# Kernel tuning notes

Measured on AMD Instinct MI355X. Metric: run time of the kernel, lower is better.

Reference implementation:

```python
import jax, jax.numpy as jnp
import numpy as np
from jax.scipy.special import logsumexp

NG, NF, NR, NW = 5, 5, 5, 4
STEP = 1 + NG + NF + NR            # 16 signatures per writer
M_OTH = NG + NF + NR               # comparisons per writer
MARGIN, RANDOM_MARGIN = 1.0, 1.5
ALPHA, BETA, P_W, R_W = 0.1, 1.0, 0.01, 0.01
GAMMA = 5.0                        # SoftDTW(gamma=5, bandwidth=int(0.1)=0 -> full DTW)
KNUM, KMUL = 5, 2.0
MAXLEN, FEAT = 512, 64
BIG = 1e10                         # finite stand-in for +inf (exp(-BIG/GAMMA) == 0 in f32)


def _pairwise_sqdist(X, Y):
    # X,Y: (B, L, F) -> (B, L, L) squared euclidean cost (SoftDTW distance func)
    xy = jnp.einsum('bif,bjf->bij', X, Y)
    d = (X * X).sum(-1)[:, :, None] + (Y * Y).sum(-1)[:, None, :] - 2.0 * xy
    return jnp.maximum(d, 0.0)


def _soft_dtw(D, la, lb):
    # Batched soft-DTW via anti-diagonal scan. Padded DP is causal, so
    # R[la, lb] only depends on D[:la, :lb]; padding never contaminates it.
    B, L, _ = D.shape
    ii = jnp.arange(1, L + 1)
    r2 = jnp.full((B, L + 1), BIG, D.dtype).at[:, 0].set(0.0)  # diag d=0: R[0,0]=0
    r1 = jnp.full((B, L + 1), BIG, D.dtype)                    # diag d=1: borders

    def step(carry, d):
        rp2, rp1 = carry
        j = d - ii
        valid = (j >= 1) & (j <= L)
        jc = jnp.clip(j, 1, L)
        Dd = D[:, ii - 1, jc - 1]                               # (B, L)
        # softmin(R[i-1,j], R[i,j-1], R[i-1,j-1]) = -g*logsumexp(-r/g)
        stack = jnp.stack([-rp1[:, :-1], -rp1[:, 1:], -rp2[:, :-1]]) / GAMMA
        smin = -GAMMA * logsumexp(stack, axis=0)
        vals = jnp.where(valid[None, :], Dd + smin, BIG)
        r_new = jnp.concatenate([jnp.full((B, 1), BIG, D.dtype), vals], axis=1)
        return (rp1, r_new), r_new

    _, R = jax.lax.scan(step, (r2, r1), jnp.arange(2, 2 * L + 1))
    # R: (2L-1, B, L+1); diag d stored at d-2, R[la, lb] sits at index la
    return R[la + lb - 2, jnp.arange(B), la]


def _mmd(src, tgt):
    # DAN-style multi-kernel gaussian MMD; signatures flattened to vectors
    b = src.shape[0]
    total = jnp.concatenate([src, tgt], axis=0)
    n = total.shape[0]
    sq = (total * total).sum(-1)
    l2 = jnp.maximum(sq[:, None] + sq[None, :] - 2.0 * (total @ total.T), 0.0)
    bw = jax.lax.stop_gradient(l2.sum()) / (n * n - n)
    bw = bw / KMUL ** (KNUM // 2)
    bws = bw * KMUL ** jnp.arange(KNUM, dtype=total.dtype)
    k = jnp.exp(-l2[None] / bws[:, None, None]).sum(0)
    return jnp.mean(k[:b, :b] + k[b:, b:] - k[:b, b:] - k[b:, :b])


def _forward(data, lens):
    w = jnp.arange(NW)
    anchor_idx = jnp.repeat(w * STEP, M_OTH)
    other_idx = (w[:, None] * STEP + 1 + jnp.arange(M_OTH)[None, :]).reshape(-1)
    D = _pairwise_sqdist(data[anchor_idx], data[other_idx])
    la, lb = lens[anchor_idx], lens[other_idx]
    r = _soft_dtw(D, la, lb)
    dists = (r / (la + lb).astype(data.dtype)).reshape(NW, M_OTH)  # avg pooling
    dist_g = dists[:, :NG]
    dist_n = dists[:, NG:]
    lk_s = jax.nn.relu(dist_g[:, :, None] + MARGIN - dist_n[:, None, :NF])
    lk_r = jax.nn.relu(dist_g[:, :, None] + RANDOM_MARGIN - dist_n[:, None, NF:])
    ca = dist_g.mean(1)
    cb = dist_n[:, :NW].mean(1)            # quirk of original: first nw negatives
    intra = (dist_g - ca[:, None]).sum(1)  # identically 0, kept for fidelity
    inter = jax.nn.relu(BETA - jnp.abs(ca - cb))
    nz_s = (lk_s > 0).sum((1, 2))
    nz_r = (lk_r > 0).sum((1, 2))
    lv = (lk_s.sum((1, 2)) + lk_r.sum((1, 2))) / (nz_s + nz_r + 1)
    # BCE over softmin pairs (dist_g[0], dist_r[j]) vs targets (1, 0):
    # softmin gives sm0 = sigmoid(dr - dg0); BCE = -(log sm0 + log(1-sm1))/2 = -log sm0
    logits = dist_n[:, NF:] - dist_g[:, 0:1]
    bce = -jnp.mean(jax.nn.log_sigmoid(logits), axis=1)
    total_loss = jnp.mean(bce + lv + intra * P_W + inter * R_W)
    # pairwise MMD over writers (i in 0..nw-1, j in 1..nw-1, i != j), nr random excluded
    pairs = np.array([(i, j) for i in range(NW) for j in range(1, NW) if i != j])
    seg = data.reshape(NW, STEP, MAXLEN, FEAT)[:, :STEP - NR]
    seg = seg.reshape(NW, STEP - NR, MAXLEN * FEAT)
    mmd_vals = jax.vmap(_mmd)(seg[pairs[:, 0]], seg[pairs[:, 1]])
    siz = NW * (NW + 1) // 2
    mmds = jnp.zeros((siz,), data.dtype).at[:pairs.shape[0]].set(mmd_vals)
    mmd1 = jnp.max(mmds) * ALPHA
    return total_loss + mmd1, nz_r.sum()


def setup_inputs():
    key = jax.random.key(0)
    k1, k2, k3 = jax.random.split(key, 3)
    data = jax.random.normal(k1, (NW * STEP, MAXLEN, FEAT), dtype=jnp.float32)
    lens = jax.random.randint(k2, (NW * STEP,), MAXLEN // 2, MAXLEN + 1, dtype=jnp.int32)
    target = jax.random.randint(k3, (NW * STEP,), 0, NW, dtype=jnp.int32)
    return {"data": data, "lens": lens, "target": target, "n_classes": 100}


def reference(data, lens, target, n_classes):
    # target / n_classes are unused in the original forward (sms is dead code)
    return _forward(data, lens)
```

## Files before the change

kernel.cpp:

```cpp
#include <hip/hip_runtime.h>
#include <math.h>

#define NG 5
#define NF 5
#define NR 5
#define NW 4
#define STEP 16
#define M_OTH 15
#define NB 60
#define L 512
#define FEAT 64
#define GAMMA 5.0f
#define SEGN 11
#define NSEG 44
#define SEGD 32768

#define C1   0.28853900817779268f
#define GLN2 3.4657359027997265f
#define BIGS 2.8853900e9f
#define BNDW 800
#define GRAM_BLK0 60
#define SENT 0x7FC000007FC00000ULL

typedef struct __align__(16) { unsigned long long x, y; } ull2_t;

__global__ __launch_bounds__(256, 2) void sqdist_kernel(const float* __restrict__ data,
                                                        const int* __restrict__ lens,
                                                        float* __restrict__ DS) {
    int b = blockIdx.z;
    int w = b / M_OTH, m = b % M_OTH;
    int la = lens[w * STEP];
    int lb = lens[w * STEP + 1 + m];
    int ti = blockIdx.y * 128;
    int tj = blockIdx.x * 128;
    if (ti >= la || tj >= lb) return;

    const float* X = data + (size_t)(w * STEP) * L * FEAT;
    const float* Y = data + (size_t)(w * STEP + 1 + m) * L * FEAT;

    __shared__ float Xs[128][68];
    __shared__ float Ys[128][68];
    __shared__ float nx[128], ny[128];

    int t = threadIdx.y * 16 + threadIdx.x;
    #pragma unroll
    for (int k = 0; k < 8; ++k) {
        int idx = t + k * 256;
        int r = idx >> 4, c = (idx & 15) * 4;
        *(float4*)&Xs[r][c] = *(const float4*)(X + (size_t)(ti + r) * FEAT + c);
        *(float4*)&Ys[r][c] = *(const float4*)(Y + (size_t)(tj + r) * FEAT + c);
    }
    __syncthreads();
    {
        int r = t & 127;
        const float* row = (t < 128) ? Xs[r] : Ys[r];
        float s = 0.f;
        #pragma unroll
        for (int f = 0; f < 64; f += 4) {
            float4 v = *(const float4*)&row[f];
            s += v.x * v.x + v.y * v.y + v.z * v.z + v.w * v.w;
        }
        if (t < 128) nx[r] = s; else ny[r] = s;
    }
    __syncthreads();

    int tx = threadIdx.x, ty = threadIdx.y;
    float acc[8][8] = {};
    for (int f = 0; f < 64; f += 4) {
        float4 xv[8], yv[8];
        #pragma unroll
        for (int a = 0; a < 8; ++a) xv[a] = *(const float4*)&Xs[16 * a + tx][f];
        #pragma unroll
        for (int c = 0; c < 8; ++c) yv[c] = *(const float4*)&Ys[16 * c + ty][f];
        #pragma unroll
        for (int a = 0; a < 8; ++a)
            #pragma unroll
            for (int c = 0; c < 8; ++c)
                acc[a][c] += xv[a].x * yv[c].x + xv[a].y * yv[c].y +
                             xv[a].z * yv[c].z + xv[a].w * yv[c].w;
    }
    #pragma unroll
    for (int a = 0; a < 8; ++a) {
        int ii = ti + 16 * a + tx;
        float xn = nx[16 * a + tx];
        #pragma unroll
        for (int c = 0; c < 8; ++c) {
            int jj = tj + 16 * c + ty;
            float d = xn + ny[16 * c + ty] - 2.0f * acc[a][c];
            size_t idx = ((size_t)b * 512 + ((jj + (ii >> 1)) & 511)) * 512 + ii;
            DS[idx] = fmaxf(d, 0.0f) * C1;
        }
    }
}

__device__ __forceinline__ float dpp_shift_up1(float x) {
    int xi = __float_as_int(x);
    int sh  = __builtin_amdgcn_update_dpp(xi, xi, 0x111, 0xF, 0xF, false);
    int b15 = __builtin_amdgcn_update_dpp(xi, xi, 0x142, 0xF, 0xF, false);
    int lane = (int)(threadIdx.x & 63);
    int r = ((lane & 15) == 0) ? b15 : sh;
    return __int_as_float(r);
}

__device__ void gram_body(const float* __restrict__ data, float* __restrict__ Gm, int f) {
    int bx = 0, rem = f;
    for (int q = 0; q < 11; ++q) { int c = 11 - q; if (rem < c) { bx = q; break; } rem -= c; }
    int by = bx + rem;
    int t = threadIdx.x;
    int lane = t & 63, wv = t >> 6;
    const float* pa[4];
    const float* pb[4];
    #pragma unroll
    for (int i = 0; i < 4; ++i) {
        int sa = bx * 4 + i;
        int sb = by * 4 + i;
        pa[i] = data + (size_t)((sa / SEGN) * STEP + (sa % SEGN)) * SEGD;
        pb[i] = data + (size_t)((sb / SEGN) * STEP + (sb % SEGN)) * SEGD;
    }
    float acc[16] = {};
    for (int d = t * 4; d < SEGD; d += 1024) {
        float4 ra[4], rb[4];
        #pragma unroll
        for (int i = 0; i < 4; ++i) ra[i] = *(const float4*)(pa[i] + d);
        #pragma unroll
        for (int i = 0; i < 4; ++i) rb[i] = *(const float4*)(pb[i] + d);
        #pragma unroll
        for (int i = 0; i < 4; ++i)
            #pragma unroll
            for (int jj = 0; jj < 4; ++jj)
                acc[i * 4 + jj] += ra[i].x * rb[jj].x + ra[i].y * rb[jj].y +
                                   ra[i].z * rb[jj].z + ra[i].w * rb[jj].w;
    }
    #pragma unroll
    for (int i = 0; i < 16; ++i)
        #pragma unroll
        for (int s = 32; s > 0; s >>= 1)
            acc[i] += __shfl_xor(acc[i], s);
    __shared__ float part[4][16];
    if (lane == 0)
        #pragma unroll
        for (int i = 0; i < 16; ++i) part[wv][i] = acc[i];
    __syncthreads();
    if (t < 16) {
        float s = part[0][t] + part[1][t] + part[2][t] + part[3][t];
        int a = bx * 4 + (t >> 2), c = by * 4 + (t & 3);
        Gm[a * NSEG + c] = s;
        Gm[c * NSEG + a] = s;
    }
}

__global__ __launch_bounds__(256) void dtw_gram_kernel(const float* __restrict__ DS,
                                                       const int* __restrict__ lens,
                                                       const float* __restrict__ data,
                                                       float* __restrict__ res,
                                                       float* __restrict__ Gm) {
    int blk = blockIdx.x;
    if (blk >= GRAM_BLK0) { gram_body(data, Gm, blk - GRAM_BLK0); return; }

    int b = blk;
    int w_ = b / M_OTH, m = b % M_OTH;
    int la = lens[w_ * STEP];
    int lb = lens[w_ * STEP + 1 + m];
    int tid = threadIdx.x;
    int W = tid >> 6, l = tid & 63, G = tid;
    const float* Db = DS + (size_t)b * 512 * 512;

    __shared__ unsigned long long bnd[3][BNDW];
    for (int k = tid; k < 3 * BNDW; k += 256)
        ((unsigned long long*)bnd)[k] = SENT;
    __syncthreads();

    int gstar = (la - 1) >> 1;
    int rstar = (la - 1) & 1;
    int tcap = lb + gstar - 1;
    if (64 * W > gstar) return;
    int gmax = min(64 * W + 63, gstar);
    int t0 = 64 * W;
    int tend = lb + gmax - 1;
    int needmax = lb + 64 * W - 1;
    bool pub = (W < 3);

    float p0 = BIGS, s0 = 1.f;
    float p1 = BIGS, s1 = 1.f;
    float pA = BIGS, sA = 1.f;
    float pC = (G == 0) ? 0.f : BIGS;
    float sC = 1.f;
    float outp = 0.f, outs = 1.f;

    float2 ring[8];
    #pragma unroll
    for (int k = 0; k < 8; ++k)
        ring[k] = *(const float2*)&Db[(size_t)((t0 + k) & 511) * 512 + 2 * G];
    unsigned long long ch[8];
    #pragma unroll
    for (int k = 0; k < 8; ++k) ch[k] = SENT;

    int j = 1 - l;
    const unsigned long long* bsrc = (W > 0) ? bnd[W - 1] : bnd[0];

    for (int t = t0; t <= tend; t += 8) {
        if (W > 0 && t <= needmax) {
            bool ok = (t + 7 <= needmax) &&
                      !__builtin_isnan(__int_as_float((int)(unsigned)ch[3])) &&
                      !__builtin_isnan(__int_as_float((int)(unsigned)ch[7]));
            if (!ok) {
                int lastIdx = min(t + 7, needmax);
                unsigned long long v = __hip_atomic_load(&bsrc[lastIdx], __ATOMIC_RELAXED,
                                                         __HIP_MEMORY_SCOPE_WORKGROUP);
                while (__builtin_isnan(__int_as_float((int)(unsigned)v))) {
                    __builtin_amdgcn_s_sleep(2);
                    v = __hip_atomic_load(&bsrc[lastIdx], __ATOMIC_RELAXED,
                                          __HIP_MEMORY_SCOPE_WORKGROUP);
                }
                __builtin_amdgcn_fence(__ATOMIC_ACQUIRE, "workgroup");
                #pragma unroll
                for (int k = 0; k < 8; ++k)
                    ch[k] = __hip_atomic_load(&bsrc[t + k], __ATOMIC_RELAXED,
                                              __HIP_MEMORY_SCOPE_WORKGROUP);
            }
        }
        #pragma unroll
        for (int k = 0; k < 8; ++k) {
            int tt = t + k;
            float l0p = BIGS, l0s = 1.0f;
            if (W > 0 && tt <= needmax) {
                l0p = __int_as_float((int)(unsigned)ch[k]);
                l0s = __int_as_float((int)(unsigned)(ch[k] >> 32));
            }
            pA = (l == 0) ? l0p : pA;
            sA = (l == 0) ? l0s : sA;
            float D0 = ring[k].x, D1 = ring[k].y;
            ring[k] = *(const float2*)&Db[(size_t)((tt + 8) & 511) * 512 + 2 * G];
            float mbc = fminf(p0, pC), xbc = fmaxf(p0, pC);
            float ebc = __builtin_amdgcn_exp2f(mbc - xbc);
            float E2  = (p0 <= pC) ? fmaf(ebc, sC, s0) : fmaf(ebc, s0, sC);
            float ref0 = fminf(pA, mbc), mx0 = fmaxf(pA, mbc);
            float e0 = __builtin_amdgcn_exp2f(ref0 - mx0);
            float s0n = (pA <= mbc) ? fmaf(e0, E2, sA) : fmaf(e0, sA, E2);
            float p0n = D0 + ref0;
            float mbc1 = fminf(p1, p0), xbc1 = fmaxf(p1, p0);
            float ebc1 = __builtin_amdgcn_exp2f(mbc1 - xbc1);
            float E2b = (p1 <= p0) ? fmaf(ebc1, s0, s1) : fmaf(ebc1, s1, s0);
            float ref1 = fminf(p0n, mbc1), mx1 = fmaxf(p0n, mbc1);
            float e1 = __builtin_amdgcn_exp2f(ref1 - mx1);
            float s1n = (p0n <= mbc1) ? fmaf(e1, E2b, s0n) : fmaf(e1, s0n, E2b);
            float p1n = D1 + ref1;
            bool valid = (unsigned)(j - 1) < (unsigned)L;
            p0 = valid ? p0n : p0;  s0 = valid ? s0n : s0;
            p1 = valid ? p1n : p1;  s1 = valid ? s1n : s1;
            if (tt == tcap) {
                if (G == gstar) { outp = rstar ? p1 : p0; outs = rstar ? s1 : s0; }
            }
            float upP = dpp_shift_up1(p1);
            float upS = dpp_shift_up1(s1);
            if (pub && l == 63) {
                union { float2 f; unsigned long long u; } pk;
                pk.f = make_float2(p1, s1);
                __hip_atomic_store(&bnd[W][tt + 1], pk.u, __ATOMIC_RELAXED,
                                   __HIP_MEMORY_SCOPE_WORKGROUP);
            }
            pC = pA; sC = sA;
            pA = upP; sA = upS;
            j += 1;
        }
        if ((t & 8) != 0) {
            p0 -= __builtin_amdgcn_logf(s0); s0 = 1.0f;
            p1 -= __builtin_amdgcn_logf(s1); s1 = 1.0f;
        }
        if (W > 0) {
            const ull2_t* sp = (const ull2_t*)&bsrc[t + 8];
            ull2_t c0 = sp[0], c1 = sp[1], c2 = sp[2], c3 = sp[3];
            ch[0] = c0.x; ch[1] = c0.y; ch[2] = c1.x; ch[3] = c1.y;
            ch[4] = c2.x; ch[5] = c2.y; ch[6] = c3.x; ch[7] = c3.y;
        }
    }
    if (G == gstar)
        res[b] = (outp - __builtin_amdgcn_logf(outs)) * GLN2 / (float)(la + lb);
}

__global__ __launch_bounds__(512) void finalize_kernel(const float* __restrict__ res,
                                                       const float* __restrict__ G,
                                                       float* __restrict__ out) {
    __shared__ float wpart[9][8];
    __shared__ float bws[9];
    __shared__ float mmds[9];
    __shared__ float wloss[NW];
    __shared__ int   wnzr[NW];
    int t = threadIdx.x, lane = t & 63, wv = t >> 6;

    if (t < NW) {
        int w = t;
        float dg[NG], dn[NF + NR];
        for (int g = 0; g < NG; ++g) dg[g] = res[w * M_OTH + g];
        for (int q2 = 0; q2 < NF + NR; ++q2) dn[q2] = res[w * M_OTH + NG + q2];
        float sum_s = 0.f, sum_r = 0.f;
        int nzs = 0, nzr = 0;
        for (int g = 0; g < NG; ++g) {
            for (int f = 0; f < NF; ++f) {
                float v = dg[g] + 1.0f - dn[f];
                if (v > 0.f) { sum_s += v; nzs++; }
            }
            for (int r = 0; r < NR; ++r) {
                float v = dg[g] + 1.5f - dn[NF + r];
                if (v > 0.f) { sum_r += v; nzr++; }
            }
        }
        float ca = (dg[0] + dg[1] + dg[2] + dg[3] + dg[4]) / 5.0f;
        float cb = (dn[0] + dn[1] + dn[2] + dn[3]) * 0.25f;
        float intra = 0.f;
        for (int g = 0; g < NG; ++g) intra += dg[g] - ca;
        float inter = fmaxf(0.f, 1.0f - fabsf(ca - cb));
        float lv = (sum_s + sum_r) / (float)(nzs + nzr + 1);
        float bce = 0.f;
        for (int r = 0; r < NR; ++r) {
            float x = dn[NF + r] - dg[0];
            float ls = (x >= 0.f) ? -log1pf(expf(-x)) : (x - log1pf(expf(x)));
            bce += ls;
        }
        bce = -bce / 5.0f;
        wloss[w] = bce + lv + intra * 0.01f + inter * 0.01f;
        wnzr[w] = nzr;
    }

    const int pi[9] = {0, 0, 0, 1, 1, 2, 2, 3, 3};
    const int pj[9] = {1, 2, 3, 2, 3, 1, 3, 1, 2};
    int pp = t / 22, qq = t % 22;
    bool act = t < 484;
    float l2v[9];
    #pragma unroll
    for (int p = 0; p < 9; ++p) {
        float v = 0.f;
        if (act) {
            int wi = pi[p], wj = pj[p];
            int gp = (pp < 11) ? wi * SEGN + pp : wj * SEGN + (pp - 11);
            int gq = (qq < 11) ? wi * SEGN + qq : wj * SEGN + (qq - 11);
            v = fmaxf(G[gp * NSEG + gp] + G[gq * NSEG + gq] - 2.f * G[gp * NSEG + gq], 0.f);
        }
        l2v[p] = v;
    }
    #pragma unroll
    for (int p = 0; p < 9; ++p) {
        float r = l2v[p];
        #pragma unroll
        for (int s = 32; s > 0; s >>= 1) r += __shfl_xor(r, s);
        if (lane == 0) wpart[p][wv] = r;
    }
    __syncthreads();
    if (t < 9) {
        float s = 0.f;
        #pragma unroll
        for (int k = 0; k < 8; ++k) s += wpart[t][k];
        bws[t] = s * (1.0f / 462.0f) * 0.25f;
    }
    __syncthreads();
    float sgn = ((pp < 11) == (qq < 11)) ? 1.f : -1.f;
    #pragma unroll
    for (int p = 0; p < 9; ++p) {
        float kv = 0.f;
        if (act) {
            float x = -l2v[p] / bws[p];
            kv = sgn * (__expf(x) + __expf(x * 0.5f) + __expf(x * 0.25f) +
                        __expf(x * 0.125f) + __expf(x * 0.0625f));
        }
        #pragma unroll
        for (int s = 32; s > 0; s >>= 1) kv += __shfl_xor(kv, s);
        if (lane == 0) wpart[p][wv] = kv;
    }
    __syncthreads();
    if (t < 9) {
        float s = 0.f;
        #pragma unroll
        for (int k = 0; k < 8; ++k) s += wpart[t][k];
        mmds[t] = s / 121.0f;
    }
    __syncthreads();
    if (t == 0) {
        float loss = 0.25f * (wloss[0] + wloss[1] + wloss[2] + wloss[3]);
        float mx = 0.f;
        for (int p = 0; p < 9; ++p) mx = fmaxf(mx, mmds[p]);
        out[0] = loss + 0.1f * mx;
        out[1] = (float)(wnzr[0] + wnzr[1] + wnzr[2] + wnzr[3]);
    }
}

extern "C" void kernel_launch(void* const* d_in, const int* in_sizes, int n_in,
                              void* d_out, int out_size, void* d_ws, size_t ws_size,
                              hipStream_t stream) {
    const float* data = (const float*)d_in[0];
    const int* lens = (const int*)d_in[1];

    float* DS  = (float*)d_ws;
    float* res = DS + (size_t)NB * 512 * 512;
    float* G   = res + 64;
    float* out = (float*)d_out;

    dim3 g1(4, 4, NB), b1(16, 16);
    sqdist_kernel<<<g1, b1, 0, stream>>>(data, lens, DS);
    dtw_gram_kernel<<<GRAM_BLK0 + 66, 256, 0, stream>>>(DS, lens, data, res, G);
    finalize_kernel<<<1, 512, 0, stream>>>(res, G, out);
}
```

Measured before the change: 185.0 us.

## Assign one DTW row per thread across eight wavefronts instead of two

The soft-DTW wavefront kernel now maps one matrix row to each thread, using 512 threads and 8 wavefronts instead of 256 threads each computing two rows. The skewed cost layout in the sqdist kernel changes to match, and the boundary-exchange buffers between wavefronts grow to 7 tiers. The gram reduction is adapted to 512 threads, and the spin-wait sleep is shortened. This halves the serial dependency chain per thread, but adds more inter-wave handoffs and pipeline fill latency and increases shared memory use.

```diff
diff --git a/kernel.cpp b/kernel.cpp
--- a/kernel.cpp
+++ b/kernel.cpp
@@ -18,7 +18,8 @@
 #define C1   0.28853900817779268f
 #define GLN2 3.4657359027997265f
 #define BIGS 2.8853900e9f
-#define BNDW 800
+#define BNDW 1056
+#define NTIER 7
 #define GRAM_BLK0 60
 #define SENT 0x7FC000007FC00000ULL
 
@@ -87,7 +88,7 @@
         for (int c = 0; c < 8; ++c) {
             int jj = tj + 16 * c + ty;
             float d = xn + ny[16 * c + ty] - 2.0f * acc[a][c];
-            size_t idx = ((size_t)b * 512 + ((jj + (ii >> 1)) & 511)) * 512 + ii;
+            size_t idx = ((size_t)b * 512 + ((jj + ii) & 511)) * 512 + ii;
             DS[idx] = fmaxf(d, 0.0f) * C1;
         }
     }
@@ -118,7 +119,7 @@
         pb[i] = data + (size_t)((sb / SEGN) * STEP + (sb % SEGN)) * SEGD;
     }
     float acc[16] = {};
-    for (int d = t * 4; d < SEGD; d += 1024) {
+    for (int d = t * 4; d < SEGD; d += 2048) {
         float4 ra[4], rb[4];
         #pragma unroll
         for (int i = 0; i < 4; ++i) ra[i] = *(const float4*)(pa[i] + d);
@@ -136,20 +137,22 @@
         #pragma unroll
         for (int s = 32; s > 0; s >>= 1)
             acc[i] += __shfl_xor(acc[i], s);
-    __shared__ float part[4][16];
+    __shared__ float part[8][16];
     if (lane == 0)
         #pragma unroll
         for (int i = 0; i < 16; ++i) part[wv][i] = acc[i];
     __syncthreads();
     if (t < 16) {
-        float s = part[0][t] + part[1][t] + part[2][t] + part[3][t];
+        float s = 0.f;
+        #pragma unroll
+        for (int k = 0; k < 8; ++k) s += part[k][t];
         int a = bx * 4 + (t >> 2), c = by * 4 + (t & 3);
         Gm[a * NSEG + c] = s;
         Gm[c * NSEG + a] = s;
     }
 }
 
-__global__ __launch_bounds__(256) void dtw_gram_kernel(const float* __restrict__ DS,
+__global__ __launch_bounds__(512) void dtw_gram_kernel(const float* __restrict__ DS,
                                                        const int* __restrict__ lens,
                                                        const float* __restrict__ data,
                                                        float* __restrict__ res,
@@ -165,37 +168,34 @@
     int W = tid >> 6, l = tid & 63, G = tid;
     const float* Db = DS + (size_t)b * 512 * 512;
 
-    __shared__ unsigned long long bnd[3][BNDW];
-    for (int k = tid; k < 3 * BNDW; k += 256)
+    __shared__ unsigned long long bnd[NTIER][BNDW];
+    for (int k = tid; k < NTIER * BNDW; k += 512)
         ((unsigned long long*)bnd)[k] = SENT;
     __syncthreads();
 
-    int gstar = (la - 1) >> 1;
-    int rstar = (la - 1) & 1;
-    int tcap = lb + gstar - 1;
+    int gstar = la - 1;
+    int tcap = la + lb - 2;
     if (64 * W > gstar) return;
     int gmax = min(64 * W + 63, gstar);
     int t0 = 64 * W;
     int tend = lb + gmax - 1;
     int needmax = lb + 64 * W - 1;
-    bool pub = (W < 3);
-
-    float p0 = BIGS, s0 = 1.f;
-    float p1 = BIGS, s1 = 1.f;
-    float pA = BIGS, sA = 1.f;
+    bool pub = (W < NTIER);
+
+    float p = BIGS, s = 1.f;
     float pC = (G == 0) ? 0.f : BIGS;
     float sC = 1.f;
+    float pA = BIGS, sA = 1.f;
     float outp = 0.f, outs = 1.f;
 
-    float2 ring[8];
+    float ring[8];
     #pragma unroll
     for (int k = 0; k < 8; ++k)
-        ring[k] = *(const float2*)&Db[(size_t)((t0 + k) & 511) * 512 + 2 * G];
+        ring[k] = Db[(size_t)(((t0 + k) & 511) * 512 + G)];
     unsigned long long ch[8];
     #pragma unroll
     for (int k = 0; k < 8; ++k) ch[k] = SENT;
 
-    int j = 1 - l;
     const unsigned long long* bsrc = (W > 0) ? bnd[W - 1] : bnd[0];
 
     for (int t = t0; t <= tend; t += 8) {
@@ -208,7 +208,7 @@
                 unsigned long long v = __hip_atomic_load(&bsrc[lastIdx], __ATOMIC_RELAXED,
                                                          __HIP_MEMORY_SCOPE_WORKGROUP);
                 while (__builtin_isnan(__int_as_float((int)(unsigned)v))) {
-                    __builtin_amdgcn_s_sleep(2);
+                    __builtin_amdgcn_s_sleep(1);
                     v = __hip_atomic_load(&bsrc[lastIdx], __ATOMIC_RELAXED,
                                           __HIP_MEMORY_SCOPE_WORKGROUP);
                 }
@@ -222,50 +222,42 @@
         #pragma unroll
         for (int k = 0; k < 8; ++k) {
             int tt = t + k;
-            float l0p = BIGS, l0s = 1.0f;
-            if (W > 0 && tt <= needmax) {
-                l0p = __int_as_float((int)(unsigned)ch[k]);
-                l0s = __int_as_float((int)(unsigned)(ch[k] >> 32));
-            }
-            pA = (l == 0) ? l0p : pA;
-            sA = (l == 0) ? l0s : sA;
-            float D0 = ring[k].x, D1 = ring[k].y;
-            ring[k] = *(const float2*)&Db[(size_t)((tt + 8) & 511) * 512 + 2 * G];
-            float mbc = fminf(p0, pC), xbc = fmaxf(p0, pC);
+            float pAx = pA, sAx = sA;
+            if (l == 0) {
+                if (W > 0) {
+                    pAx = __int_as_float((int)(unsigned)ch[k]);
+                    sAx = __int_as_float((int)(unsigned)(ch[k] >> 32));
+                } else { pAx = BIGS; sAx = 1.f; }
+            }
+            float D = ring[k];
+            ring[k] = Db[(size_t)((((tt + 8) & 511)) * 512 + G)];
+            float mbc = fminf(p, pC), xbc = fmaxf(p, pC);
             float ebc = __builtin_amdgcn_exp2f(mbc - xbc);
-            float E2  = (p0 <= pC) ? fmaf(ebc, sC, s0) : fmaf(ebc, s0, sC);
-            float ref0 = fminf(pA, mbc), mx0 = fmaxf(pA, mbc);
-            float e0 = __builtin_amdgcn_exp2f(ref0 - mx0);
-            float s0n = (pA <= mbc) ? fmaf(e0, E2, sA) : fmaf(e0, sA, E2);
-            float p0n = D0 + ref0;
-            float mbc1 = fminf(p1, p0), xbc1 = fmaxf(p1, p0);
-            float ebc1 = __builtin_amdgcn_exp2f(mbc1 - xbc1);
-            float E2b = (p1 <= p0) ? fmaf(ebc1, s0, s1) : fmaf(ebc1, s1, s0);
-            float ref1 = fminf(p0n, mbc1), mx1 = fmaxf(p0n, mbc1);
-            float e1 = __builtin_amdgcn_exp2f(ref1 - mx1);
-            float s1n = (p0n <= mbc1) ? fmaf(e1, E2b, s0n) : fmaf(e1, s0n, E2b);
-            float p1n = D1 + ref1;
-            bool valid = (unsigned)(j - 1) < (unsigned)L;
-            p0 = valid ? p0n : p0;  s0 = valid ? s0n : s0;
-            p1 = valid ? p1n : p1;  s1 = valid ? s1n : s1;
+            float E2  = (p <= pC) ? fmaf(ebc, sC, s) : fmaf(ebc, s, sC);
+            float ref = fminf(pAx, mbc), mx = fmaxf(pAx, mbc);
+            float e = __builtin_amdgcn_exp2f(ref - mx);
+            float sN = (pAx <= mbc) ? fmaf(e, E2, sAx) : fmaf(e, sAx, E2);
+            float pN = D + ref;
+            bool valid = (tt >= G);
+            p = valid ? pN : p;
+            s = valid ? sN : s;
             if (tt == tcap) {
-                if (G == gstar) { outp = rstar ? p1 : p0; outs = rstar ? s1 : s0; }
-            }
-            float upP = dpp_shift_up1(p1);
-            float upS = dpp_shift_up1(s1);
+                if (G == gstar) { outp = p; outs = s; }
+            }
+            float upP = dpp_shift_up1(p);
+            float upS = dpp_shift_up1(s);
             if (pub && l == 63) {
                 union { float2 f; unsigned long long u; } pk;
-                pk.f = make_float2(p1, s1);
+                pk.f = make_float2(p, s);
                 __hip_atomic_store(&bnd[W][tt + 1], pk.u, __ATOMIC_RELAXED,
                                    __HIP_MEMORY_SCOPE_WORKGROUP);
             }
-            pC = pA; sC = sA;
+            pC = pAx; sC = sAx;
             pA = upP; sA = upS;
-            j += 1;
         }
         if ((t & 8) != 0) {
-            p0 -= __builtin_amdgcn_logf(s0); s0 = 1.0f;
-            p1 -= __builtin_amdgcn_logf(s1); s1 = 1.0f;
+            p -= __builtin_amdgcn_logf(s);
+            s = 1.0f;
         }
         if (W > 0) {
             const ull2_t* sp = (const ull2_t*)&bsrc[t + 8];
@@ -396,6 +388,6 @@
 
     dim3 g1(4, 4, NB), b1(16, 16);
     sqdist_kernel<<<g1, b1, 0, stream>>>(data, lens, DS);
-    dtw_gram_kernel<<<GRAM_BLK0 + 66, 256, 0, stream>>>(DS, lens, data, res, G);
+    dtw_gram_kernel<<<GRAM_BLK0 + 66, 512, 0, stream>>>(DS, lens, data, res, G);
     finalize_kernel<<<1, 512, 0, stream>>>(res, G, out);
 }
```

Result: slower. 201.5 us (+8.9%).

## Tile soft-DTW wavefront into 2x4 cell blocks per thread with packed DS layout

Applied to the files above, without the earlier changes.

Each thread now computes a 2-row by 4-column block of DP cells per step instead of a 2x1 column. The wavefront advances in column groups of four, which cuts the number of outer steps and the DPP shifts and inter-wave boundary exchanges per cell. The sqdist output is rearranged so each thread loads two float4s per step. The softmin now uses a three-way exp form and rescales every step. The risk is higher register pressure and more exp instructions per cell.

```diff
diff --git a/kernel.cpp b/kernel.cpp
--- a/kernel.cpp
+++ b/kernel.cpp
@@ -18,11 +18,9 @@
 #define C1   0.28853900817779268f
 #define GLN2 3.4657359027997265f
 #define BIGS 2.8853900e9f
-#define BNDW 800
+#define BNDK 136
 #define GRAM_BLK0 60
-#define SENT 0x7FC000007FC00000ULL
-
-typedef struct __align__(16) { unsigned long long x, y; } ull2_t;
+#define DSTRIDE 262144
 
 __global__ __launch_bounds__(256, 2) void sqdist_kernel(const float* __restrict__ data,
                                                         const int* __restrict__ lens,
@@ -79,28 +77,39 @@
                 acc[a][c] += xv[a].x * yv[c].x + xv[a].y * yv[c].y +
                              xv[a].z * yv[c].z + xv[a].w * yv[c].w;
     }
+    size_t base = (size_t)b * DSTRIDE;
     #pragma unroll
     for (int a = 0; a < 8; ++a) {
         int ii = ti + 16 * a + tx;
         float xn = nx[16 * a + tx];
+        int G = ii >> 1;
         #pragma unroll
         for (int c = 0; c < 8; ++c) {
             int jj = tj + 16 * c + ty;
             float d = xn + ny[16 * c + ty] - 2.0f * acc[a][c];
-            size_t idx = ((size_t)b * 512 + ((jj + (ii >> 1)) & 511)) * 512 + ii;
-            DS[idx] = fmaxf(d, 0.0f) * C1;
-        }
-    }
-}
-
-__device__ __forceinline__ float dpp_shift_up1(float x) {
+            int slot = ((jj >> 2) + G) & 127;
+            int inner = ((jj & 3) << 1) | (ii & 1);
+            DS[base + (size_t)slot * 2048 + G * 8 + inner] = fmaxf(d, 0.0f) * C1;
+        }
+    }
+}
+
+__device__ __forceinline__ float dpp_up(float x, bool rh) {
     int xi = __float_as_int(x);
     int sh  = __builtin_amdgcn_update_dpp(xi, xi, 0x111, 0xF, 0xF, false);
     int b15 = __builtin_amdgcn_update_dpp(xi, xi, 0x142, 0xF, 0xF, false);
-    int lane = (int)(threadIdx.x & 63);
-    int r = ((lane & 15) == 0) ? b15 : sh;
-    return __int_as_float(r);
-}
+    return __int_as_float(rh ? b15 : sh);
+}
+
+#define CELL(qp, qs, pa, sa, pb, sb, pc, sc, Dv)                          \
+    {                                                                     \
+        float ref = fminf(fminf((pa), (pb)), (pc));                       \
+        float eA = __builtin_amdgcn_exp2f(ref - (pa));                    \
+        float eB = __builtin_amdgcn_exp2f(ref - (pb));                    \
+        float eC = __builtin_amdgcn_exp2f(ref - (pc));                    \
+        qs = fmaf(eA, (sa), fmaf(eB, (sb), eC * (sc)));                   \
+        qp = (Dv) + ref;                                                  \
+    }
 
 __device__ void gram_body(const float* __restrict__ data, float* __restrict__ Gm, int f) {
     int bx = 0, rem = f;
@@ -163,115 +172,150 @@
     int lb = lens[w_ * STEP + 1 + m];
     int tid = threadIdx.x;
     int W = tid >> 6, l = tid & 63, G = tid;
-    const float* Db = DS + (size_t)b * 512 * 512;
-
-    __shared__ unsigned long long bnd[3][BNDW];
-    for (int k = tid; k < 3 * BNDW; k += 256)
-        ((unsigned long long*)bnd)[k] = SENT;
+    bool rh = ((l & 15) == 0);
+    const float* dsb = DS + (size_t)b * DSTRIDE;
+
+    __shared__ float bndF[3][BNDK * 8];
+    for (int k = tid; k < 3 * BNDK * 8; k += 256)
+        ((float*)bndF)[k] = __int_as_float(0x7FC00000);
     __syncthreads();
 
     int gstar = (la - 1) >> 1;
     int rstar = (la - 1) & 1;
-    int tcap = lb + gstar - 1;
+    int kcap  = (lb - 1) >> 2;
+    int cstar = (lb - 1) & 3;
+    int tcap  = kcap + gstar;
     if (64 * W > gstar) return;
     int gmax = min(64 * W + 63, gstar);
     int t0 = 64 * W;
-    int tend = lb + gmax - 1;
-    int needmax = lb + 64 * W - 1;
-    bool pub = (W < 3);
+    int tend = kcap + gmax;
+    bool pubw = (W < 3);
 
     float p0 = BIGS, s0 = 1.f;
     float p1 = BIGS, s1 = 1.f;
-    float pA = BIGS, sA = 1.f;
     float pC = (G == 0) ? 0.f : BIGS;
     float sC = 1.f;
-    float outp = 0.f, outs = 1.f;
-
-    float2 ring[8];
-    #pragma unroll
-    for (int k = 0; k < 8; ++k)
-        ring[k] = *(const float2*)&Db[(size_t)((t0 + k) & 511) * 512 + 2 * G];
-    unsigned long long ch[8];
-    #pragma unroll
-    for (int k = 0; k < 8; ++k) ch[k] = SENT;
-
-    int j = 1 - l;
-    const unsigned long long* bsrc = (W > 0) ? bnd[W - 1] : bnd[0];
-
-    for (int t = t0; t <= tend; t += 8) {
-        if (W > 0 && t <= needmax) {
-            bool ok = (t + 7 <= needmax) &&
-                      !__builtin_isnan(__int_as_float((int)(unsigned)ch[3])) &&
-                      !__builtin_isnan(__int_as_float((int)(unsigned)ch[7]));
-            if (!ok) {
-                int lastIdx = min(t + 7, needmax);
-                unsigned long long v = __hip_atomic_load(&bsrc[lastIdx], __ATOMIC_RELAXED,
-                                                         __HIP_MEMORY_SCOPE_WORKGROUP);
-                while (__builtin_isnan(__int_as_float((int)(unsigned)v))) {
-                    __builtin_amdgcn_s_sleep(2);
-                    v = __hip_atomic_load(&bsrc[lastIdx], __ATOMIC_RELAXED,
+    float outp = BIGS, outs = 1.f;
+
+    float4 ringA[4], ringB[4];
+    #pragma unroll
+    for (int kk = 0; kk < 4; ++kk) {
+        const float* pp = dsb + (size_t)((t0 + kk) & 127) * 2048 + G * 8;
+        ringA[kk] = *(const float4*)pp;
+        ringB[kk] = *(const float4*)(pp + 4);
+    }
+    float4 chA[4], chB[4];
+    if (W == 0) {
+        #pragma unroll
+        for (int kk = 0; kk < 4; ++kk) {
+            chA[kk] = make_float4(BIGS, 1.f, BIGS, 1.f);
+            chB[kk] = make_float4(BIGS, 1.f, BIGS, 1.f);
+        }
+    } else {
+        const float* src = &bndF[W - 1][0];
+        #pragma unroll
+        for (int kk = 0; kk < 4; ++kk) {
+            chA[kk] = *(const float4*)(src + kk * 8);
+            chB[kk] = *(const float4*)(src + kk * 8 + 4);
+        }
+    }
+    float nxP0 = BIGS, nxS0 = 1.f, nxP1 = BIGS, nxS1 = 1.f;
+    float nxP2 = BIGS, nxS2 = 1.f, nxP3 = BIGS, nxS3 = 1.f;
+    bool isl0 = (l == 0);
+
+    for (int tbase = t0; tbase <= tend; tbase += 4) {
+        int kb = tbase - 64 * W;
+        if (W > 0 && kb <= kcap) {
+            int vidx = min(kb + 3, kcap);
+            const float* vp  = &bndF[W - 1][vidx * 8 + 6];
+            const float* src = &bndF[W - 1][(size_t)kb * 8];
+            for (;;) {
+                float chk = 0.f;
+                #pragma unroll
+                for (int kk = 0; kk < 4; ++kk) {
+                    if (kb + kk <= kcap)
+                        chk += chA[kk].x + chA[kk].y + chA[kk].z + chA[kk].w +
+                               chB[kk].x + chB[kk].y + chB[kk].z + chB[kk].w;
+                }
+                if (!__builtin_isnan(chk)) break;
+                float v = __hip_atomic_load(vp, __ATOMIC_RELAXED,
+                                            __HIP_MEMORY_SCOPE_WORKGROUP);
+                while (__builtin_isnan(v)) {
+                    __builtin_amdgcn_s_sleep(1);
+                    v = __hip_atomic_load(vp, __ATOMIC_RELAXED,
                                           __HIP_MEMORY_SCOPE_WORKGROUP);
                 }
                 __builtin_amdgcn_fence(__ATOMIC_ACQUIRE, "workgroup");
                 #pragma unroll
-                for (int k = 0; k < 8; ++k)
-                    ch[k] = __hip_atomic_load(&bsrc[t + k], __ATOMIC_RELAXED,
-                                              __HIP_MEMORY_SCOPE_WORKGROUP);
-            }
-        }
-        #pragma unroll
-        for (int k = 0; k < 8; ++k) {
-            int tt = t + k;
-            float l0p = BIGS, l0s = 1.0f;
-            if (W > 0 && tt <= needmax) {
-                l0p = __int_as_float((int)(unsigned)ch[k]);
-                l0s = __int_as_float((int)(unsigned)(ch[k] >> 32));
-            }
-            pA = (l == 0) ? l0p : pA;
-            sA = (l == 0) ? l0s : sA;
-            float D0 = ring[k].x, D1 = ring[k].y;
-            ring[k] = *(const float2*)&Db[(size_t)((tt + 8) & 511) * 512 + 2 * G];
-            float mbc = fminf(p0, pC), xbc = fmaxf(p0, pC);
-            float ebc = __builtin_amdgcn_exp2f(mbc - xbc);
-            float E2  = (p0 <= pC) ? fmaf(ebc, sC, s0) : fmaf(ebc, s0, sC);
-            float ref0 = fminf(pA, mbc), mx0 = fmaxf(pA, mbc);
-            float e0 = __builtin_amdgcn_exp2f(ref0 - mx0);
-            float s0n = (pA <= mbc) ? fmaf(e0, E2, sA) : fmaf(e0, sA, E2);
-            float p0n = D0 + ref0;
-            float mbc1 = fminf(p1, p0), xbc1 = fmaxf(p1, p0);
-            float ebc1 = __builtin_amdgcn_exp2f(mbc1 - xbc1);
-            float E2b = (p1 <= p0) ? fmaf(ebc1, s0, s1) : fmaf(ebc1, s1, s0);
-            float ref1 = fminf(p0n, mbc1), mx1 = fmaxf(p0n, mbc1);
-            float e1 = __builtin_amdgcn_exp2f(ref1 - mx1);
-            float s1n = (p0n <= mbc1) ? fmaf(e1, E2b, s0n) : fmaf(e1, s0n, E2b);
-            float p1n = D1 + ref1;
-            bool valid = (unsigned)(j - 1) < (unsigned)L;
-            p0 = valid ? p0n : p0;  s0 = valid ? s0n : s0;
-            p1 = valid ? p1n : p1;  s1 = valid ? s1n : s1;
+                for (int kk = 0; kk < 4; ++kk) {
+                    chA[kk] = *(const float4*)(src + kk * 8);
+                    chB[kk] = *(const float4*)(src + kk * 8 + 4);
+                }
+            }
+        }
+        #pragma unroll
+        for (int kk = 0; kk < 4; ++kk) {
+            int tt = tbase + kk;
+            bool act = (tt >= G);
+            float4 Da = ringA[kk], Dbv = ringB[kk];
+            {
+                const float* pp = dsb + (size_t)((tt + 4) & 127) * 2048 + G * 8;
+                ringA[kk] = *(const float4*)pp;
+                ringB[kk] = *(const float4*)(pp + 4);
+            }
+            float iP0 = isl0 ? chA[kk].x : nxP0, iS0 = isl0 ? chA[kk].y : nxS0;
+            float iP1 = isl0 ? chA[kk].z : nxP1, iS1 = isl0 ? chA[kk].w : nxS1;
+            float iP2 = isl0 ? chB[kk].x : nxP2, iS2 = isl0 ? chB[kk].y : nxS2;
+            float iP3 = isl0 ? chB[kk].z : nxP3, iS3 = isl0 ? chB[kk].w : nxS3;
+            float q0p, q0s, q1p, q1s, q2p, q2s, q3p, q3s;
+            float q4p, q4s, q5p, q5s, q6p, q6s, q7p, q7s;
+            CELL(q0p, q0s, iP0, iS0, p0, s0, pC, sC, Da.x);
+            CELL(q1p, q1s, q0p, q0s, p1, s1, p0, s0, Da.y);
+            CELL(q2p, q2s, iP1, iS1, q0p, q0s, iP0, iS0, Da.z);
+            CELL(q3p, q3s, q2p, q2s, q1p, q1s, q0p, q0s, Da.w);
+            CELL(q4p, q4s, iP2, iS2, q2p, q2s, iP1, iS1, Dbv.x);
+            CELL(q5p, q5s, q4p, q4s, q3p, q3s, q2p, q2s, Dbv.y);
+            CELL(q6p, q6s, iP3, iS3, q4p, q4s, iP2, iS2, Dbv.z);
+            CELL(q7p, q7s, q6p, q6s, q5p, q5s, q4p, q4s, Dbv.w);
             if (tt == tcap) {
-                if (G == gstar) { outp = rstar ? p1 : p0; outs = rstar ? s1 : s0; }
-            }
-            float upP = dpp_shift_up1(p1);
-            float upS = dpp_shift_up1(s1);
-            if (pub && l == 63) {
-                union { float2 f; unsigned long long u; } pk;
-                pk.f = make_float2(p1, s1);
-                __hip_atomic_store(&bnd[W][tt + 1], pk.u, __ATOMIC_RELAXED,
-                                   __HIP_MEMORY_SCOPE_WORKGROUP);
-            }
-            pC = pA; sC = sA;
-            pA = upP; sA = upS;
-            j += 1;
-        }
-        if ((t & 8) != 0) {
-            p0 -= __builtin_amdgcn_logf(s0); s0 = 1.0f;
-            p1 -= __builtin_amdgcn_logf(s1); s1 = 1.0f;
-        }
+                if (G == gstar) {
+                    int sel = (cstar << 1) | rstar;
+                    float cp, cs;
+                    if (sel == 0)      { cp = q0p; cs = q0s; }
+                    else if (sel == 1) { cp = q1p; cs = q1s; }
+                    else if (sel == 2) { cp = q2p; cs = q2s; }
+                    else if (sel == 3) { cp = q3p; cs = q3s; }
+                    else if (sel == 4) { cp = q4p; cs = q4s; }
+                    else if (sel == 5) { cp = q5p; cs = q5s; }
+                    else if (sel == 6) { cp = q6p; cs = q6s; }
+                    else               { cp = q7p; cs = q7s; }
+                    outp = cp; outs = cs;
+                }
+            }
+            p0 = act ? q6p : p0;  s0 = act ? q6s : s0;
+            p1 = act ? q7p : p1;  s1 = act ? q7s : s1;
+            pC = act ? iP3 : pC;  sC = act ? iS3 : sC;
+            if (pubw && l == 63 && act) {
+                int k63 = tt - G;
+                float* dst = &bndF[W][(size_t)k63 * 8];
+                *(float4*)dst       = make_float4(q1p, q1s, q3p, q3s);
+                *(float4*)(dst + 4) = make_float4(q5p, q5s, q7p, q7s);
+            }
+            nxP0 = dpp_up(q1p, rh); nxS0 = dpp_up(q1s, rh);
+            nxP1 = dpp_up(q3p, rh); nxS1 = dpp_up(q3s, rh);
+            nxP2 = dpp_up(q5p, rh); nxS2 = dpp_up(q5s, rh);
+            nxP3 = dpp_up(q7p, rh); nxS3 = dpp_up(q7s, rh);
+        }
+        p0 -= __builtin_amdgcn_logf(s0); s0 = 1.f;
+        p1 -= __builtin_amdgcn_logf(s1); s1 = 1.f;
         if (W > 0) {
-            const ull2_t* sp = (const ull2_t*)&bsrc[t + 8];
-            ull2_t c0 = sp[0], c1 = sp[1], c2 = sp[2], c3 = sp[3];
-            ch[0] = c0.x; ch[1] = c0.y; ch[2] = c1.x; ch[3] = c1.y;
-            ch[4] = c2.x; ch[5] = c2.y; ch[6] = c3.x; ch[7] = c3.y;
+            int sb_ = min(kb + 4, BNDK - 4);
+            const float* src = &bndF[W - 1][(size_t)sb_ * 8];
+            #pragma unroll
+            for (int kk = 0; kk < 4; ++kk) {
+                chA[kk] = *(const float4*)(src + kk * 8);
+                chB[kk] = *(const float4*)(src + kk * 8 + 4);
+            }
         }
     }
     if (G == gstar)
@@ -390,7 +434,7 @@
     const int* lens = (const int*)d_in[1];
 
     float* DS  = (float*)d_ws;
-    float* res = DS + (size_t)NB * 512 * 512;
+    float* res = DS + (size_t)NB * DSTRIDE;
     float* G   = res + 64;
     float* out = (float*)d_out;
 
```

New measurement: 203.4 us. 10.0% more time.
